# Kernel tuning notes

Hardware: AMD Instinct MI355X
Metric: run time of the kernel (lower is better)

Reference implementation:

```python
import jax, jax.numpy as jnp
import numpy as np

N = 50000      # nodes
E = 800000     # edges (avg degree 16)
D = 64         # emb_dim
L = 5          # num_layer
BN_EPS = 1e-5


def setup_inputs() -> dict:
    key = jax.random.key(0)
    ks = jax.random.split(key, 10)
    x = jax.random.randint(ks[0], (N,), 0, 1)                      # indices into 1-row embedding
    edge_index = jax.random.randint(ks[1], (2, E), 0, N)
    edge_attr = jax.random.normal(ks[2], (E, 7), dtype=jnp.float32)
    s = lambda k, shape: (jax.random.normal(k, shape, dtype=jnp.float32) * 0.05)
    node_emb = s(ks[3], (1, D))
    # per-layer GINConv params, stacked on a leading layer axis for lax.scan
    We = s(ks[4], (L, 7, D));   be = jnp.zeros((L, D), jnp.float32)      # edge_encoder
    eps = jnp.zeros((L,), jnp.float32)                                   # GIN eps
    W1 = s(ks[5], (L, D, 2 * D)); b1 = jnp.zeros((L, 2 * D), jnp.float32)  # mlp linear1
    g1 = jnp.ones((L, 2 * D), jnp.float32); bb1 = jnp.zeros((L, 2 * D), jnp.float32)  # mlp BN
    W2 = s(ks[6], (L, 2 * D, D)); b2 = jnp.zeros((L, D), jnp.float32)    # mlp linear2
    g2 = jnp.ones((L, D), jnp.float32); bb2 = jnp.zeros((L, D), jnp.float32)  # outer BN
    return dict(x=x, edge_index=edge_index, edge_attr=edge_attr, node_emb=node_emb,
                We=We, be=be, eps=eps, W1=W1, b1=b1, g1=g1, bb1=bb1,
                W2=W2, b2=b2, g2=g2, bb2=bb2)


def _bn(a, g, b):
    # BatchNorm1d in training mode: batch statistics over node axis, biased var
    m = a.mean(axis=0)
    v = jnp.var(a, axis=0)
    return (a - m) * jax.lax.rsqrt(v + BN_EPS) * g + b


def reference(x, edge_index, edge_attr, node_emb, We, be, eps,
              W1, b1, g1, bb1, W2, b2, g2, bb2):
    src, dst = edge_index[0], edge_index[1]
    h = node_emb[x]                                    # [N, D]
    relu_flags = jnp.arange(L) < (L - 1)               # ReLU on all but last layer

    def step(h, p):
        We_, be_, eps_, W1_, b1_, g1_, bb1_, W2_, b2_, g2_, bb2_, flag = p
        ee = edge_attr @ We_ + be_                     # [E, D] edge embeddings
        msg = jax.nn.relu(h[src] + ee)                 # gather + elementwise
        agg = jax.ops.segment_sum(msg, dst, num_segments=N)  # scatter-add
        z = (1.0 + eps_) * h + agg                     # GIN combine
        a = jax.nn.relu(_bn(z @ W1_ + b1_, g1_, bb1_)) # mlp: lin -> BN -> ReLU
        hb = _bn(a @ W2_ + b2_, g2_, bb2_)             # lin -> outer BN
        h_new = jnp.where(flag, jax.nn.relu(hb), hb)   # dropout omitted (eval)
        return h_new, None

    h, _ = jax.lax.scan(step, h, (We, be, eps, W1, b1, g1, bb1, W2, b2, g2, bb2, relu_flags))
    return h                                           # JK='last'
```

## Files before the change

### kernel.cpp

```cpp
#include <hip/hip_runtime.h>
#include <hip/hip_fp16.h>

#define NN 50000
#define EE 800000
#define NB 782

typedef _Float16 f16x8 __attribute__((ext_vector_type(8)));
typedef _Float16 f16x4 __attribute__((ext_vector_type(4)));
typedef _Float16 f16x2 __attribute__((ext_vector_type(2)));
typedef float f32x4 __attribute__((ext_vector_type(4)));

__device__ __forceinline__ unsigned h2u(__half2 h) {
    union { __half2 h; unsigned u; } c; c.h = h; return c.u;
}
__device__ __forceinline__ f16x2 u2h(unsigned u) {
    union { unsigned u; f16x2 h; } c; c.u = u; return c.h;
}

__global__ __launch_bounds__(256) void hist_kernel(const int* __restrict__ ei,
                                                   int* __restrict__ deg) {
    const int e = (blockIdx.x << 8) + threadIdx.x;
    atomicAdd(&deg[ei[EE + e]], 1);
}

__global__ __launch_bounds__(256) void scanA_kernel(const int* __restrict__ deg,
                                                    int* __restrict__ bsum) {
    __shared__ int sm[256];
    const int t = threadIdx.x;
    const int i = (blockIdx.x << 8) + t;
    sm[t] = (i < NN) ? deg[i] : 0;
    __syncthreads();
    for (int o = 128; o > 0; o >>= 1) {
        if (t < o) sm[t] += sm[t + o];
        __syncthreads();
    }
    if (t == 0) bsum[blockIdx.x] = sm[0];
}

__global__ __launch_bounds__(256) void scanB_kernel(int* __restrict__ bsum) {
    __shared__ int sm[256];
    const int t = threadIdx.x;
    const int v = (t < 196) ? bsum[t] : 0;
    sm[t] = v;
    __syncthreads();
    for (int o = 1; o < 256; o <<= 1) {
        const int u = (t >= o) ? sm[t - o] : 0;
        __syncthreads();
        sm[t] += u;
        __syncthreads();
    }
    bsum[t] = sm[t] - v;
}

__global__ __launch_bounds__(256) void scanC_kernel(const int* __restrict__ deg,
                                                    const int* __restrict__ bsum,
                                                    int* __restrict__ off,
                                                    int* __restrict__ cur) {
    __shared__ int sm[256];
    const int t = threadIdx.x;
    const int i = (blockIdx.x << 8) + t;
    const int v = (i < NN) ? deg[i] : 0;
    sm[t] = v;
    __syncthreads();
    for (int o = 1; o < 256; o <<= 1) {
        const int u = (t >= o) ? sm[t - o] : 0;
        __syncthreads();
        sm[t] += u;
        __syncthreads();
    }
    const int excl = bsum[blockIdx.x] + sm[t] - v;
    if (i < NN) { off[i] = excl; cur[i] = excl; }
    else if (i == NN) off[NN] = excl;
}

__global__ __launch_bounds__(256) void scatter_kernel(const int* __restrict__ ei,
                                                      const float* __restrict__ ea,
                                                      int* __restrict__ cur,
                                                      int4* __restrict__ pea) {
    const int e = (blockIdx.x << 8) + threadIdx.x;
    const int src = ei[e];
    const int dst = ei[EE + e];
    const float* a = ea + e * 7;
    const unsigned h0 = __half_as_ushort(__float2half(a[0]));
    const unsigned h1 = __half_as_ushort(__float2half(a[1]));
    const unsigned h2 = __half_as_ushort(__float2half(a[2]));
    const unsigned h3 = __half_as_ushort(__float2half(a[3]));
    const unsigned h4 = __half_as_ushort(__float2half(a[4]));
    const unsigned h5 = __half_as_ushort(__float2half(a[5]));
    const unsigned h6 = __half_as_ushort(__float2half(a[6]));
    const int pos = atomicAdd(&cur[dst], 1);
    pea[pos] = make_int4((int)(h0 | (h1 << 16)), (int)(h2 | (h3 << 16)),
                         (int)(h4 | (h5 << 16)), (int)(h6 | ((unsigned)src << 16)));
}

__global__ __launch_bounds__(256) void bnstats_kernel(
    const float* __restrict__ part, const int nb, const int half,
    const float* __restrict__ g, const float* __restrict__ bb,
    float* __restrict__ scsh)
{
    __shared__ float ss[256], qq[256];
    const int c = blockIdx.x, t = threadIdx.x;
    const int stride = half << 1;
    float s = 0.f, q = 0.f;
    for (int b = t; b < nb; b += 256) {
        s += part[b * stride + c];
        q += part[b * stride + half + c];
    }
    ss[t] = s; qq[t] = q;
    __syncthreads();
    for (int o = 128; o > 0; o >>= 1) {
        if (t < o) { ss[t] += ss[t + o]; qq[t] += qq[t + o]; }
        __syncthreads();
    }
    if (t == 0) {
        const float m = ss[0] * (1.0f / NN);
        const float v = fmaxf(qq[0] * (1.0f / NN) - m * m, 0.0f);
        const float sc = g[c] * rsqrtf(v + 1e-5f);
        scsh[c] = sc;
        scsh[half + c] = bb[c] - m * sc;
    }
}

__global__ __launch_bounds__(256) void wprep_kernel(
    const float* __restrict__ W1, const float* __restrict__ W2,
    const float* __restrict__ We, const float* __restrict__ be,
    _Float16* __restrict__ W1s, _Float16* __restrict__ W2s,
    unsigned* __restrict__ Wepk, unsigned* __restrict__ be2)
{
    const int i = (blockIdx.x << 8) + threadIdx.x;
    if (i < 40960) {
        const int l = i >> 13, j = i & 8191, k = j >> 7, n = j & 127;
        W1s[(l << 13) + ((((k >> 3) << 7) + n) << 3) + (k & 7)] = (_Float16)W1[i];
    } else if (i < 81920) {
        const int i2 = i - 40960;
        const int l = i2 >> 13, j = i2 & 8191, k = j >> 6, n = j & 63;
        W2s[(l << 13) + ((((k >> 3) << 6) + n) << 3) + (k & 7)] = (_Float16)W2[i2];
    } else if (i < 83040) {
        const int i3 = i - 81920;
        const int l = i3 / 224;
        const int r = i3 - l * 224;
        const int k = r >> 5, s = r & 31;
        const float* W = We + l * 448 + (k << 6) + (s << 1);
        Wepk[i3] = h2u(__floats2half2_rn(W[0], W[1]));
    } else if (i < 83200) {
        const int i4 = i - 83040;
        const int l = i4 >> 5, s = i4 & 31;
        const float* B = be + (l << 6) + (s << 1);
        be2[i4] = h2u(__floats2half2_rn(B[0], B[1]));
    }
}

__global__ __launch_bounds__(256) void hprep_kernel(
    const float* __restrict__ y2, const float* __restrict__ scsh2,
    __half* __restrict__ h16)
{
    const int i4 = (blockIdx.x << 8) + threadIdx.x;
    const float4 v = ((const float4*)y2)[i4];
    const int d0 = (i4 << 2) & 63;
    const float a = fmaxf(fmaf(v.x, scsh2[d0 + 0], scsh2[64 + d0 + 0]), 0.f);
    const float b = fmaxf(fmaf(v.y, scsh2[d0 + 1], scsh2[64 + d0 + 1]), 0.f);
    const float c = fmaxf(fmaf(v.z, scsh2[d0 + 2], scsh2[64 + d0 + 2]), 0.f);
    const float d = fmaxf(fmaf(v.w, scsh2[d0 + 3], scsh2[64 + d0 + 3]), 0.f);
    *(int2*)(h16 + (i4 << 2)) =
        make_int2((int)h2u(__floats2half2_rn(a, b)),
                  (int)h2u(__floats2half2_rn(c, d)));
}

__global__ __launch_bounds__(256) void hprep0_kernel(
    const int* __restrict__ x, const float* __restrict__ nemb,
    __half* __restrict__ h16)
{
    const int i4 = (blockIdx.x << 8) + threadIdx.x;
    const int n = i4 >> 4;
    const float4 v = ((const float4*)nemb)[(x[n] << 4) + (i4 & 15)];
    *(int2*)(h16 + (i4 << 2)) =
        make_int2((int)h2u(__floats2half2_rn(v.x, v.y)),
                  (int)h2u(__floats2half2_rn(v.z, v.w)));
}

__global__ __launch_bounds__(256) void gather_kernel(
    const int* __restrict__ off, const int4* __restrict__ pea,
    const unsigned* __restrict__ h32,
    const unsigned* __restrict__ Wepk, const unsigned* __restrict__ be2,
    const float* __restrict__ epsp,
    unsigned* __restrict__ z32)
{
    const int t = threadIdx.x;
    const int lane = t & 63;
    const int s = lane & 31;
    const int n = (blockIdx.x << 3) + ((t >> 6) << 1) + (lane >> 5);

    const f16x2 w0 = u2h(Wepk[s]),       w1 = u2h(Wepk[32 + s]),
                w2 = u2h(Wepk[64 + s]),  w3 = u2h(Wepk[96 + s]),
                w4 = u2h(Wepk[128 + s]), w5 = u2h(Wepk[160 + s]),
                w6 = u2h(Wepk[192 + s]);
    const f16x2 beh = u2h(be2[s]);

    const int e0 = off[n], e1 = off[n + 1];
    const int deg = e1 - e0;
    const int degMax = max(deg, __shfl_xor(deg, 32));

    float aLo = 0.f, aHi = 0.f;
    for (int i = 0; i < degMax; i += 8) {
        int4 pk[8]; int vld[8];
#pragma unroll
        for (int j = 0; j < 8; ++j) {
            const int ej = e0 + i + j;
            vld[j] = (ej < e1);
            pk[j] = pea[vld[j] ? ej : 0];
        }
        unsigned hv[8];
#pragma unroll
        for (int j = 0; j < 8; ++j) {
            const int src = (int)(((unsigned)pk[j].w) >> 16);
            hv[j] = h32[(src << 5) + s];
        }
#pragma unroll
        for (int j = 0; j < 8; ++j) {
            const f16x2 a01 = u2h((unsigned)pk[j].x);
            const f16x2 a23 = u2h((unsigned)pk[j].y);
            const f16x2 a45 = u2h((unsigned)pk[j].z);
            const f16x2 a6x = u2h((unsigned)pk[j].w);
            f16x2 ee = beh;
            ee += (f16x2){a01[0], a01[0]} * w0;
            ee += (f16x2){a01[1], a01[1]} * w1;
            ee += (f16x2){a23[0], a23[0]} * w2;
            ee += (f16x2){a23[1], a23[1]} * w3;
            ee += (f16x2){a45[0], a45[0]} * w4;
            ee += (f16x2){a45[1], a45[1]} * w5;
            ee += (f16x2){a6x[0], a6x[0]} * w6;
            f16x2 m2 = u2h(hv[j]) + ee;
            const _Float16 zz = (_Float16)0.f;
            m2 = (f16x2){ m2[0] > zz ? m2[0] : zz, m2[1] > zz ? m2[1] : zz };
            const float mf = vld[j] ? 1.f : 0.f;
            aLo = fmaf(mf, (float)m2[0], aLo);
            aHi = fmaf(mf, (float)m2[1], aHi);
        }
    }
    const f16x2 hn2 = u2h(h32[(n << 5) + s]);
    const float e1f = 1.0f + epsp[0];
    const float zLo = fmaf(e1f, (float)hn2[0], aLo);
    const float zHi = fmaf(e1f, (float)hn2[1], aHi);
    z32[(n << 5) + s] = h2u(__floats2half2_rn(zLo, zHi));
}

__global__ __launch_bounds__(256) void mm1_kernel(
    const _Float16* __restrict__ z16, const _Float16* __restrict__ W1s,
    const float* __restrict__ b1p, _Float16* __restrict__ y1h,
    float* __restrict__ part1)
{
    __shared__ float smS[4][128], smQ[4][128];
    const int t = threadIdx.x;
    const int wv = t >> 6, lane = t & 63;
    const int q = lane >> 4, ln = lane & 15;
    const int r0 = blockIdx.x << 6;

    const int rowm = r0 + (wv << 4) + ln;
    const f16x8 af0 = *(const f16x8*)(z16 + rowm * 64 + (q << 3));
    const f16x8 af1 = *(const f16x8*)(z16 + rowm * 64 + 32 + (q << 3));

    f32x4 acc[8];
#pragma unroll
    for (int n0 = 0; n0 < 8; ++n0) acc[n0] = (f32x4){0.f, 0.f, 0.f, 0.f};
#pragma unroll
    for (int n0 = 0; n0 < 8; ++n0) {
        const f16x8 bf0 = *(const f16x8*)(W1s + (((q << 7) + (n0 << 4) + ln) << 3));
        const f16x8 bf1 = *(const f16x8*)(W1s + ((((4 + q) << 7) + (n0 << 4) + ln) << 3));
        acc[n0] = __builtin_amdgcn_mfma_f32_16x16x32_f16(af0, bf0, acc[n0], 0, 0, 0);
        acc[n0] = __builtin_amdgcn_mfma_f32_16x16x32_f16(af1, bf1, acc[n0], 0, 0, 0);
    }

    const int baseRow = r0 + (wv << 4) + (q << 2);
#pragma unroll
    for (int n0 = 0; n0 < 8; ++n0) {
        const int col = (n0 << 4) + ln;
        const float bb = b1p[col];
        float s = 0.f, sq = 0.f;
#pragma unroll
        for (int rg = 0; rg < 4; ++rg) {
            const int row = baseRow + rg;
            const float y = acc[n0][rg] + bb;
            y1h[row * 128 + col] = (_Float16)y;
            const float m = (row < NN) ? 1.f : 0.f;
            s = fmaf(m, y, s); sq = fmaf(m, y * y, sq);
        }
        s += __shfl_xor(s, 16); s += __shfl_xor(s, 32);
        sq += __shfl_xor(sq, 16); sq += __shfl_xor(sq, 32);
        if (lane < 16) { smS[wv][col] = s; smQ[wv][col] = sq; }
    }
    __syncthreads();
    if (t < 128) {
        const float s = smS[0][t] + smS[1][t] + smS[2][t] + smS[3][t];
        const float q2 = smQ[0][t] + smQ[1][t] + smQ[2][t] + smQ[3][t];
        part1[(blockIdx.x << 8) + t] = s;
        part1[(blockIdx.x << 8) + 128 + t] = q2;
    }
}

__global__ __launch_bounds__(256) void mm2_kernel(
    const _Float16* __restrict__ y1h, const float* __restrict__ scsh1,
    const _Float16* __restrict__ W2s, const float* __restrict__ b2,
    float* __restrict__ y2, float* __restrict__ part2)
{
    __shared__ float smS[4][64], smQ[4][64];
    const int t = threadIdx.x;
    const int wv = t >> 6, lane = t & 63;
    const int q = lane >> 4, ln = lane & 15;
    const int r0 = blockIdx.x << 6;

    const int rowm = r0 + (wv << 4) + ln;
    f16x8 af[4];
#pragma unroll
    for (int ks = 0; ks < 4; ++ks) {
        const int k0 = (ks << 5) + (q << 3);
        const f16x8 raw = *(const f16x8*)(y1h + rowm * 128 + k0);
        const float4 scA = *(const float4*)(scsh1 + k0);
        const float4 scB = *(const float4*)(scsh1 + k0 + 4);
        const float4 shA = *(const float4*)(scsh1 + 128 + k0);
        const float4 shB = *(const float4*)(scsh1 + 128 + k0 + 4);
        const float sc[8] = {scA.x, scA.y, scA.z, scA.w, scB.x, scB.y, scB.z, scB.w};
        const float sh[8] = {shA.x, shA.y, shA.z, shA.w, shB.x, shB.y, shB.z, shB.w};
        f16x8 a;
#pragma unroll
        for (int j = 0; j < 8; ++j)
            a[j] = (_Float16)fmaxf(fmaf((float)raw[j], sc[j], sh[j]), 0.f);
        af[ks] = a;
    }

    f32x4 acc[4];
#pragma unroll
    for (int n0 = 0; n0 < 4; ++n0) acc[n0] = (f32x4){0.f, 0.f, 0.f, 0.f};
#pragma unroll
    for (int n0 = 0; n0 < 4; ++n0) {
#pragma unroll
        for (int ks = 0; ks < 4; ++ks) {
            const f16x8 bf = *(const f16x8*)(
                W2s + (((((ks << 2) + q) << 6) + (n0 << 4) + ln) << 3));
            acc[n0] = __builtin_amdgcn_mfma_f32_16x16x32_f16(af[ks], bf, acc[n0], 0, 0, 0);
        }
    }

    const int baseRow = r0 + (wv << 4) + (q << 2);
#pragma unroll
    for (int n0 = 0; n0 < 4; ++n0) {
        const int col = (n0 << 4) + ln;
        const float bb = b2[col];
        float s = 0.f, sq = 0.f;
#pragma unroll
        for (int rg = 0; rg < 4; ++rg) {
            const int row = baseRow + rg;
            const float y = acc[n0][rg] + bb;
            y2[row * 64 + col] = y;
            const float m = (row < NN) ? 1.f : 0.f;
            s = fmaf(m, y, s); sq = fmaf(m, y * y, sq);
        }
        s += __shfl_xor(s, 16); s += __shfl_xor(s, 32);
        sq += __shfl_xor(sq, 16); sq += __shfl_xor(sq, 32);
        if (lane < 16) { smS[wv][col] = s; smQ[wv][col] = sq; }
    }
    __syncthreads();
    if (t < 64) {
        const float s = smS[0][t] + smS[1][t] + smS[2][t] + smS[3][t];
        const float q2 = smQ[0][t] + smQ[1][t] + smQ[2][t] + smQ[3][t];
        part2[(blockIdx.x << 7) + t] = s;
        part2[(blockIdx.x << 7) + 64 + t] = q2;
    }
}

__global__ __launch_bounds__(256) void final_kernel(
    const float* __restrict__ y2, const float* __restrict__ scsh2,
    float* __restrict__ out)
{
    const int i = (blockIdx.x << 8) + threadIdx.x;
    if (i >= NN * 64) return;
    const int d = i & 63;
    out[i] = fmaf(y2[i], scsh2[d], scsh2[64 + d]);
}

extern "C" void kernel_launch(void* const* d_in, const int* in_sizes, int n_in,
                              void* d_out, int out_size, void* d_ws, size_t ws_size,
                              hipStream_t stream)
{
    const int*   x    = (const int*)d_in[0];
    const int*   ei   = (const int*)d_in[1];
    const float* ea   = (const float*)d_in[2];
    const float* nemb = (const float*)d_in[3];
    const float* We   = (const float*)d_in[4];
    const float* be   = (const float*)d_in[5];
    const float* eps  = (const float*)d_in[6];
    const float* W1   = (const float*)d_in[7];
    const float* b1   = (const float*)d_in[8];
    const float* g1   = (const float*)d_in[9];
    const float* bb1  = (const float*)d_in[10];
    const float* W2   = (const float*)d_in[11];
    const float* b2   = (const float*)d_in[12];
    const float* g2   = (const float*)d_in[13];
    const float* bb2  = (const float*)d_in[14];
    float* out = (float*)d_out;

    int*      iws   = (int*)d_ws;
    float*    fws   = (float*)d_ws;
    int*      off   = iws + 0;
    int*      deg   = iws + 50048;
    int*      cur   = iws + 100096;
    int*      bsum  = iws + 150144;
    float*    scsh1 = fws + 150400;
    float*    scsh2 = fws + 150656;
    float*    part1 = fws + 150784;
    float*    part2 = fws + 350976;
    _Float16* W1s   = (_Float16*)(fws + 451072);
    _Float16* W2s   = (_Float16*)(fws + 471552);
    unsigned* Wepk  = (unsigned*)(fws + 492032);
    unsigned* be2   = (unsigned*)(fws + 493152);
    int4*     pea   = (int4*)(iws + 493312);
    _Float16* z16   = (_Float16*)(fws + 3693312);
    _Float16* y1h   = (_Float16*)(fws + 5294848);
    float*    y2    = fws + 5294848;
    __half*   h16   = (__half*)(fws + 8497920);

    hipMemsetAsync(deg, 0, 50000 * sizeof(int), stream);

    hist_kernel   <<<3125, 256, 0, stream>>>(ei, deg);
    scanA_kernel  <<<196,  256, 0, stream>>>(deg, bsum);
    scanB_kernel  <<<1,    256, 0, stream>>>(bsum);
    scanC_kernel  <<<196,  256, 0, stream>>>(deg, bsum, off, cur);
    scatter_kernel<<<3125, 256, 0, stream>>>(ei, ea, cur, pea);
    wprep_kernel  <<<325,  256, 0, stream>>>(W1, W2, We, be, W1s, W2s, Wepk, be2);
    hprep0_kernel <<<3125, 256, 0, stream>>>(x, nemb, h16);

    for (int l = 0; l < 5; ++l) {
        gather_kernel<<<6250, 256, 0, stream>>>(
            off, pea, (const unsigned*)h16, Wepk + l * 224, be2 + l * 32,
            eps + l, (unsigned*)z16);

        mm1_kernel<<<NB, 256, 0, stream>>>(z16, W1s + l * 8192, b1 + l * 128,
                                           y1h, part1);

        bnstats_kernel<<<128, 256, 0, stream>>>(part1, NB, 128,
                                                g1 + l * 128, bb1 + l * 128, scsh1);

        mm2_kernel<<<NB, 256, 0, stream>>>(y1h, scsh1, W2s + l * 8192, b2 + l * 64,
                                           y2, part2);

        bnstats_kernel<<<64, 256, 0, stream>>>(part2, NB, 64,
                                               g2 + l * 64, bb2 + l * 64, scsh2);

        if (l < 4)
            hprep_kernel<<<3125, 256, 0, stream>>>(y2, scsh2, h16);
    }

    final_kernel<<<12500, 256, 0, stream>>>(y2, scsh2, out);
}
```

Before: 490.5 us.

## Split node features into two 32-dim halves and gather each half separately

Stores node features and GIN combine outputs as two separate 32-column half-precision arrays and runs the edge gather kernel twice per layer, once per half, with 16 lanes per node. The aim is to shrink the randomly gathered feature table per pass so it stays resident in cache. In exchange, the packed edge records are streamed twice and the edge embedding is recomputed, and each gathered row segment is only 64 bytes.

```diff
diff --git a/kernel.cpp b/kernel.cpp
--- a/kernel.cpp
+++ b/kernel.cpp
@@ -152,56 +152,62 @@
 
 __global__ __launch_bounds__(256) void hprep_kernel(
     const float* __restrict__ y2, const float* __restrict__ scsh2,
-    __half* __restrict__ h16)
+    unsigned* __restrict__ hA, unsigned* __restrict__ hB)
 {
     const int i4 = (blockIdx.x << 8) + threadIdx.x;
     const float4 v = ((const float4*)y2)[i4];
     const int d0 = (i4 << 2) & 63;
+    const int n = i4 >> 4;
     const float a = fmaxf(fmaf(v.x, scsh2[d0 + 0], scsh2[64 + d0 + 0]), 0.f);
     const float b = fmaxf(fmaf(v.y, scsh2[d0 + 1], scsh2[64 + d0 + 1]), 0.f);
     const float c = fmaxf(fmaf(v.z, scsh2[d0 + 2], scsh2[64 + d0 + 2]), 0.f);
     const float d = fmaxf(fmaf(v.w, scsh2[d0 + 3], scsh2[64 + d0 + 3]), 0.f);
-    *(int2*)(h16 + (i4 << 2)) =
-        make_int2((int)h2u(__floats2half2_rn(a, b)),
-                  (int)h2u(__floats2half2_rn(c, d)));
+    unsigned* p = (d0 < 32) ? hA : hB;
+    const int w = (n << 4) + ((d0 & 31) >> 1);
+    p[w] = h2u(__floats2half2_rn(a, b));
+    p[w + 1] = h2u(__floats2half2_rn(c, d));
 }
 
 __global__ __launch_bounds__(256) void hprep0_kernel(
     const int* __restrict__ x, const float* __restrict__ nemb,
-    __half* __restrict__ h16)
+    unsigned* __restrict__ hA, unsigned* __restrict__ hB)
 {
     const int i4 = (blockIdx.x << 8) + threadIdx.x;
     const int n = i4 >> 4;
+    const int d0 = (i4 << 2) & 63;
     const float4 v = ((const float4*)nemb)[(x[n] << 4) + (i4 & 15)];
-    *(int2*)(h16 + (i4 << 2)) =
-        make_int2((int)h2u(__floats2half2_rn(v.x, v.y)),
-                  (int)h2u(__floats2half2_rn(v.z, v.w)));
+    unsigned* p = (d0 < 32) ? hA : hB;
+    const int w = (n << 4) + ((d0 & 31) >> 1);
+    p[w] = h2u(__floats2half2_rn(v.x, v.y));
+    p[w + 1] = h2u(__floats2half2_rn(v.z, v.w));
 }
 
 __global__ __launch_bounds__(256) void gather_kernel(
     const int* __restrict__ off, const int4* __restrict__ pea,
-    const unsigned* __restrict__ h32,
-    const unsigned* __restrict__ Wepk, const unsigned* __restrict__ be2,
+    const unsigned* __restrict__ hp,
+    const unsigned* __restrict__ Wp,
+    const unsigned* __restrict__ bep,
     const float* __restrict__ epsp,
-    unsigned* __restrict__ z32)
+    unsigned* __restrict__ zp)
 {
     const int t = threadIdx.x;
     const int lane = t & 63;
-    const int s = lane & 31;
-    const int n = (blockIdx.x << 3) + ((t >> 6) << 1) + (lane >> 5);
-
-    const f16x2 w0 = u2h(Wepk[s]),       w1 = u2h(Wepk[32 + s]),
-                w2 = u2h(Wepk[64 + s]),  w3 = u2h(Wepk[96 + s]),
-                w4 = u2h(Wepk[128 + s]), w5 = u2h(Wepk[160 + s]),
-                w6 = u2h(Wepk[192 + s]);
-    const f16x2 beh = u2h(be2[s]);
+    const int s = lane & 15;
+    const int n = (blockIdx.x << 4) + (((t >> 6) << 2) | (lane >> 4));
+
+    const f16x2 w0 = u2h(Wp[s]),        w1 = u2h(Wp[32 + s]),
+                w2 = u2h(Wp[64 + s]),   w3 = u2h(Wp[96 + s]),
+                w4 = u2h(Wp[128 + s]),  w5 = u2h(Wp[160 + s]),
+                w6 = u2h(Wp[192 + s]);
+    const f16x2 beh = u2h(bep[s]);
 
     const int e0 = off[n], e1 = off[n + 1];
     const int deg = e1 - e0;
-    const int degMax = max(deg, __shfl_xor(deg, 32));
+    int dm = max(deg, __shfl_xor(deg, 16));
+    dm = max(dm, __shfl_xor(dm, 32));
 
     float aLo = 0.f, aHi = 0.f;
-    for (int i = 0; i < degMax; i += 8) {
+    for (int i = 0; i < dm; i += 8) {
         int4 pk[8]; int vld[8];
 #pragma unroll
         for (int j = 0; j < 8; ++j) {
@@ -213,7 +219,7 @@
 #pragma unroll
         for (int j = 0; j < 8; ++j) {
             const int src = (int)(((unsigned)pk[j].w) >> 16);
-            hv[j] = h32[(src << 5) + s];
+            hv[j] = hp[(src << 4) + s];
         }
 #pragma unroll
         for (int j = 0; j < 8; ++j) {
@@ -237,15 +243,16 @@
             aHi = fmaf(mf, (float)m2[1], aHi);
         }
     }
-    const f16x2 hn2 = u2h(h32[(n << 5) + s]);
+    const f16x2 hn2 = u2h(hp[(n << 4) + s]);
     const float e1f = 1.0f + epsp[0];
     const float zLo = fmaf(e1f, (float)hn2[0], aLo);
     const float zHi = fmaf(e1f, (float)hn2[1], aHi);
-    z32[(n << 5) + s] = h2u(__floats2half2_rn(zLo, zHi));
+    zp[(n << 4) + s] = h2u(__floats2half2_rn(zLo, zHi));
 }
 
 __global__ __launch_bounds__(256) void mm1_kernel(
-    const _Float16* __restrict__ z16, const _Float16* __restrict__ W1s,
+    const _Float16* __restrict__ zA, const _Float16* __restrict__ zB,
+    const _Float16* __restrict__ W1s,
     const float* __restrict__ b1p, _Float16* __restrict__ y1h,
     float* __restrict__ part1)
 {
@@ -256,8 +263,8 @@
     const int r0 = blockIdx.x << 6;
 
     const int rowm = r0 + (wv << 4) + ln;
-    const f16x8 af0 = *(const f16x8*)(z16 + rowm * 64 + (q << 3));
-    const f16x8 af1 = *(const f16x8*)(z16 + rowm * 64 + 32 + (q << 3));
+    const f16x8 af0 = *(const f16x8*)(zA + rowm * 32 + (q << 3));
+    const f16x8 af1 = *(const f16x8*)(zB + rowm * 32 + (q << 3));
 
     f32x4 acc[8];
 #pragma unroll
@@ -413,10 +420,12 @@
     unsigned* Wepk  = (unsigned*)(fws + 492032);
     unsigned* be2   = (unsigned*)(fws + 493152);
     int4*     pea   = (int4*)(iws + 493312);
-    _Float16* z16   = (_Float16*)(fws + 3693312);
+    unsigned* zA    = (unsigned*)(fws + 3693312);
+    unsigned* zB    = (unsigned*)(fws + 4494080);
     _Float16* y1h   = (_Float16*)(fws + 5294848);
     float*    y2    = fws + 5294848;
-    __half*   h16   = (__half*)(fws + 8497920);
+    unsigned* hA    = (unsigned*)(fws + 8497920);
+    unsigned* hB    = (unsigned*)(fws + 9297920);
 
     hipMemsetAsync(deg, 0, 50000 * sizeof(int), stream);
 
@@ -426,15 +435,16 @@
     scanC_kernel  <<<196,  256, 0, stream>>>(deg, bsum, off, cur);
     scatter_kernel<<<3125, 256, 0, stream>>>(ei, ea, cur, pea);
     wprep_kernel  <<<325,  256, 0, stream>>>(W1, W2, We, be, W1s, W2s, Wepk, be2);
-    hprep0_kernel <<<3125, 256, 0, stream>>>(x, nemb, h16);
+    hprep0_kernel <<<3125, 256, 0, stream>>>(x, nemb, hA, hB);
 
     for (int l = 0; l < 5; ++l) {
-        gather_kernel<<<6250, 256, 0, stream>>>(
-            off, pea, (const unsigned*)h16, Wepk + l * 224, be2 + l * 32,
-            eps + l, (unsigned*)z16);
-
-        mm1_kernel<<<NB, 256, 0, stream>>>(z16, W1s + l * 8192, b1 + l * 128,
-                                           y1h, part1);
+        gather_kernel<<<3125, 256, 0, stream>>>(
+            off, pea, hA, Wepk + l * 224, be2 + l * 32, eps + l, zA);
+        gather_kernel<<<3125, 256, 0, stream>>>(
+            off, pea, hB, Wepk + l * 224 + 16, be2 + l * 32 + 16, eps + l, zB);
+
+        mm1_kernel<<<NB, 256, 0, stream>>>((const _Float16*)zA, (const _Float16*)zB,
+                                           W1s + l * 8192, b1 + l * 128, y1h, part1);
 
         bnstats_kernel<<<128, 256, 0, stream>>>(part1, NB, 128,
                                                 g1 + l * 128, bb1 + l * 128, scsh1);
@@ -446,7 +456,7 @@
                                                g2 + l * 64, bb2 + l * 64, scsh2);
 
         if (l < 4)
-            hprep_kernel<<<3125, 256, 0, stream>>>(y2, scsh2, h16);
+            hprep_kernel<<<3125, 256, 0, stream>>>(y2, scsh2, hA, hB);
     }
 
     final_kernel<<<12500, 256, 0, stream>>>(y2, scsh2, out);
```

Result: slower. 521.7 us (+6.4%).

## Pad CSR segments to multiples of eight with sentinel edges; accumulate in half

Applied to the files above, without the earlier changes.

Each node's edge segment in the CSR is rounded up to a multiple of 8. A new fill kernel writes dummy packed edges that point at a sentinel node NN, whose feature row is set to a large negative half value so the ReLU message becomes zero. This lets the gather loop drop the per-edge validity checks, the masked FMAs and the cross-half-wave degMax shuffle. Messages are now summed in packed f16 instead of f32, which cuts conversions but risks losing accuracy on high-degree nodes. The workspace offsets move to make room for the larger padded edge array.

```diff
diff --git a/kernel.cpp b/kernel.cpp
--- a/kernel.cpp
+++ b/kernel.cpp
@@ -28,7 +28,7 @@
     __shared__ int sm[256];
     const int t = threadIdx.x;
     const int i = (blockIdx.x << 8) + t;
-    sm[t] = (i < NN) ? deg[i] : 0;
+    sm[t] = (i < NN) ? ((deg[i] + 7) & ~7) : 0;
     __syncthreads();
     for (int o = 128; o > 0; o >>= 1) {
         if (t < o) sm[t] += sm[t + o];
@@ -59,7 +59,7 @@
     __shared__ int sm[256];
     const int t = threadIdx.x;
     const int i = (blockIdx.x << 8) + t;
-    const int v = (i < NN) ? deg[i] : 0;
+    const int v = (i < NN) ? ((deg[i] + 7) & ~7) : 0;
     sm[t] = v;
     __syncthreads();
     for (int o = 1; o < 256; o <<= 1) {
@@ -91,6 +91,19 @@
     const int pos = atomicAdd(&cur[dst], 1);
     pea[pos] = make_int4((int)(h0 | (h1 << 16)), (int)(h2 | (h3 << 16)),
                          (int)(h4 | (h5 << 16)), (int)(h6 | ((unsigned)src << 16)));
+}
+
+__global__ __launch_bounds__(256) void fill_kernel(
+    const int* __restrict__ off, const int* __restrict__ cur,
+    int4* __restrict__ pea, unsigned* __restrict__ h32)
+{
+    const int i = (blockIdx.x << 8) + threadIdx.x;
+    if (i < 32) h32[(NN << 5) + i] = 0xFBFFFBFFu;
+    if (i >= NN * 8) return;
+    const int n = i >> 3, j = i & 7;
+    const int pos = cur[n] + j;
+    if (pos < off[n + 1])
+        pea[pos] = make_int4(0, 0, 0, (int)(((unsigned)NN) << 16));
 }
 
 __global__ __launch_bounds__(256) void bnstats_kernel(
@@ -197,18 +210,12 @@
     const f16x2 beh = u2h(be2[s]);
 
     const int e0 = off[n], e1 = off[n + 1];
-    const int deg = e1 - e0;
-    const int degMax = max(deg, __shfl_xor(deg, 32));
-
-    float aLo = 0.f, aHi = 0.f;
-    for (int i = 0; i < degMax; i += 8) {
-        int4 pk[8]; int vld[8];
-#pragma unroll
-        for (int j = 0; j < 8; ++j) {
-            const int ej = e0 + i + j;
-            vld[j] = (ej < e1);
-            pk[j] = pea[vld[j] ? ej : 0];
-        }
+
+    f16x2 acc2 = (f16x2){(_Float16)0.f, (_Float16)0.f};
+    for (int e = e0; e < e1; e += 8) {
+        int4 pk[8];
+#pragma unroll
+        for (int j = 0; j < 8; ++j) pk[j] = pea[e + j];
         unsigned hv[8];
 #pragma unroll
         for (int j = 0; j < 8; ++j) {
@@ -232,15 +239,13 @@
             f16x2 m2 = u2h(hv[j]) + ee;
             const _Float16 zz = (_Float16)0.f;
             m2 = (f16x2){ m2[0] > zz ? m2[0] : zz, m2[1] > zz ? m2[1] : zz };
-            const float mf = vld[j] ? 1.f : 0.f;
-            aLo = fmaf(mf, (float)m2[0], aLo);
-            aHi = fmaf(mf, (float)m2[1], aHi);
+            acc2 += m2;
         }
     }
     const f16x2 hn2 = u2h(h32[(n << 5) + s]);
     const float e1f = 1.0f + epsp[0];
-    const float zLo = fmaf(e1f, (float)hn2[0], aLo);
-    const float zHi = fmaf(e1f, (float)hn2[1], aHi);
+    const float zLo = fmaf(e1f, (float)hn2[0], (float)acc2[0]);
+    const float zHi = fmaf(e1f, (float)hn2[1], (float)acc2[1]);
     z32[(n << 5) + s] = h2u(__floats2half2_rn(zLo, zHi));
 }
 
@@ -413,10 +418,10 @@
     unsigned* Wepk  = (unsigned*)(fws + 492032);
     unsigned* be2   = (unsigned*)(fws + 493152);
     int4*     pea   = (int4*)(iws + 493312);
-    _Float16* z16   = (_Float16*)(fws + 3693312);
-    _Float16* y1h   = (_Float16*)(fws + 5294848);
-    float*    y2    = fws + 5294848;
-    __half*   h16   = (__half*)(fws + 8497920);
+    _Float16* z16   = (_Float16*)(fws + 5093312);
+    _Float16* y1h   = (_Float16*)(fws + 6694848);
+    float*    y2    = fws + 6694848;
+    __half*   h16   = (__half*)(fws + 9897920);
 
     hipMemsetAsync(deg, 0, 50000 * sizeof(int), stream);
 
@@ -425,6 +430,7 @@
     scanB_kernel  <<<1,    256, 0, stream>>>(bsum);
     scanC_kernel  <<<196,  256, 0, stream>>>(deg, bsum, off, cur);
     scatter_kernel<<<3125, 256, 0, stream>>>(ei, ea, cur, pea);
+    fill_kernel   <<<1563, 256, 0, stream>>>(off, cur, pea, (unsigned*)h16);
     wprep_kernel  <<<325,  256, 0, stream>>>(W1, W2, We, be, W1s, W2s, Wepk, be2);
     hprep0_kernel <<<3125, 256, 0, stream>>>(x, nemb, h16);
 
```

Result: no change. 486.5 us (-0.8%).
